# Performance work log

Measured on AMD Instinct MI355X. Metric: run time of the kernel, lower is better.

The kernel has to match this reference:

```python
import jax, jax.numpy as jnp
import numpy as np

B, T = 8, 4096
H, V, K = 512, 32000, 9


def setup_inputs() -> dict:
    key = jax.random.key(0)
    k1, k2, k3 = jax.random.split(key, 3)
    x = jax.random.randint(k1, (B, T), 0, V, dtype=jnp.int32)
    # conv1d weight [out_ch=H, in_ch=V, K], xavier-like scale
    scale = 1.0 / np.sqrt(V * K)
    W = jax.random.normal(k2, (H, V, K), dtype=jnp.float32) * scale
    b = jax.random.normal(k3, (H,), dtype=jnp.float32) * 0.01
    return {"x": x, "W": W, "b": b}


def reference(x, W, b):
    """one_hot(x, V) -> conv1d(V->H, K, pad=K//2) expressed as gather+sum.

    out[b,t,c] = bias[c] + sum_k W[c, x[b, t+k-pad], k]  (zero outside [0,T)).
    """
    Bx, Tx = x.shape
    Hh, Vv, Kk = W.shape
    pad = Kk // 2
    t = jnp.arange(Tx)
    acc = jnp.zeros((Bx, Tx, Hh), dtype=W.dtype)
    for k in range(Kk):  # small fixed kernel loop (K=9)
        src = t + (k - pad)                      # [T]
        valid = (src >= 0) & (src < Tx)          # [T]
        src_c = jnp.clip(src, 0, Tx - 1)
        ids = x[:, src_c]                        # [B,T]
        emb = jnp.take(W[:, :, k].T, ids, axis=0)  # [B,T,H] gather of column k
        acc = acc + jnp.where(valid[None, :, None], emb, jnp.zeros((), W.dtype))
    return acc + b  # [B,T,H]
```

## Files before the change

### kernel.cpp

```cpp
#include <hip/hip_runtime.h>
#include <hip/hip_bf16.h>


#define Hc 512
#define Vc 32000
#define Kc 9
#define Tc 4096
#define Bc 8
#define Mc (Vc * Kc)
#define ROWU ((Kc * Hc) / 2)
#define T_TILE 32

__device__ __forceinline__ unsigned short f2bf(float f) {
  unsigned int u = __float_as_uint(f);
  u += 0x7FFFu + ((u >> 16) & 1u);
  return (unsigned short)(u >> 16);
}

__global__ __launch_bounds__(256) void wt_transpose_kernel(
    const float* __restrict__ in, unsigned short* __restrict__ out) {
  __shared__ float tile[64][65];
  const int m0 = blockIdx.x * 64;
  const int c0 = blockIdx.y * 64;
  const int tx = threadIdx.x & 63;
  const int ty = threadIdx.x >> 6;
#pragma unroll
  for (int r = 0; r < 16; ++r) {
    const int row = ty * 16 + r;
    tile[row][tx] = in[(size_t)(c0 + row) * Mc + (m0 + tx)];
  }
  __syncthreads();
#pragma unroll
  for (int r = 0; r < 16; ++r) {
    const int mrow = ty * 16 + r;
    out[(size_t)(m0 + mrow) * Hc + (c0 + tx)] = f2bf(tile[tx][mrow]);
  }
}

__global__ __launch_bounds__(256) void conv_gather_kernel(
    const int* __restrict__ x, const unsigned int* __restrict__ Wt,
    const float* __restrict__ bias, float* __restrict__ out) {
  __shared__ int ids[T_TILE + Kc - 1];
  const int blk = blockIdx.x;
  const int b = blk >> 7;
  const int t0 = (blk & 127) * T_TILE;
  const int tid = threadIdx.x;
  if (tid < T_TILE + Kc - 1) {
    const int s = t0 + tid - (Kc / 2);
    ids[tid] = (s >= 0 && s < Tc) ? x[b * Tc + s] : Vc;
  }
  __syncthreads();
  const float2 b2 = *(const float2*)(bias + 2 * tid);
  float2* out2 = (float2*)out;
  for (int tt = 0; tt < T_TILE; ++tt) {
    float2 acc = b2;
#pragma unroll
    for (int k = 0; k < Kc; ++k) {
      const int id = ids[tt + k];
      const unsigned int w = Wt[(size_t)id * ROWU + k * (Hc / 2) + tid];
      acc.x += __uint_as_float(w << 16);
      acc.y += __uint_as_float(w & 0xFFFF0000u);
    }
    out2[(size_t)(b * Tc + t0 + tt) * (Hc / 2) + tid] = acc;
  }
}

__global__ __launch_bounds__(256) void conv_fallback_kernel(
    const int* __restrict__ x, const float* __restrict__ W,
    const float* __restrict__ bias, float* __restrict__ out) {
  const size_t idx = (size_t)blockIdx.x * 256 + threadIdx.x;
  const int c = (int)(idx & (Hc - 1));
  const size_t bt = idx >> 9;
  const int t = (int)(bt & (Tc - 1));
  const int b = (int)(bt >> 12);
  float acc = bias[c];
#pragma unroll
  for (int k = 0; k < Kc; ++k) {
    const int s = t + k - (Kc / 2);
    if (s >= 0 && s < Tc) {
      const int id = x[b * Tc + s];
      acc += W[(size_t)c * Mc + (size_t)id * Kc + k];
    }
  }
  out[idx] = acc;
}

extern "C" void kernel_launch(void* const* d_in, const int* in_sizes, int n_in,
                              void* d_out, int out_size, void* d_ws, size_t ws_size,
                              hipStream_t stream) {
  const int* x = (const int*)d_in[0];
  const float* W = (const float*)d_in[1];
  const float* bias = (const float*)d_in[2];
  float* out = (float*)d_out;

  const size_t wt_bytes = (size_t)(Vc + 1) * Kc * Hc * 2;
  if (ws_size >= wt_bytes) {
    unsigned short* Wt = (unsigned short*)d_ws;
    hipMemsetAsync(Wt + (size_t)Vc * Kc * Hc, 0, (size_t)Kc * Hc * 2, stream);
    dim3 g1(Mc / 64, Hc / 64);
    wt_transpose_kernel<<<g1, 256, 0, stream>>>(W, Wt);
    conv_gather_kernel<<<Bc * (Tc / T_TILE), 256, 0, stream>>>(
        x, (const unsigned int*)Wt, bias, out);
  } else {
    const size_t n = (size_t)Bc * Tc * Hc;
    conv_fallback_kernel<<<(int)(n / 256), 256, 0, stream>>>(x, W, bias, out);
  }
}
```

Before: 238.6 us.

## Compact transposed weights to only vocabulary ids present in input

Adds a marking pass that assigns a compact slot to each vocabulary id appearing in x, with slot 0 reserved as a zero row. The transpose kernel still reads all of W but writes bf16-packed rows only for used ids, and the gather kernel looks up ids through the slot table. The goal is to cut the write traffic of the transposed buffer and make the gathered rows denser in cache. This adds an atomic pass and extra memsets, and the mark kernel's race handling (a sentinel value followed by a plain store) relies on ordering between kernel launches.

```diff
diff --git a/kernel.cpp b/kernel.cpp
--- a/kernel.cpp
+++ b/kernel.cpp
@@ -10,6 +10,7 @@
 #define Mc (Vc * Kc)
 #define ROWU ((Kc * Hc) / 2)
 #define T_TILE 32
+#define WT_ROWS (Vc + 1)
 
 __device__ __forceinline__ unsigned short f2bf(float f) {
   unsigned int u = __float_as_uint(f);
@@ -17,8 +18,18 @@
   return (unsigned short)(u >> 16);
 }
 
+__global__ __launch_bounds__(256) void mark_kernel(
+    const int* __restrict__ x, int* __restrict__ slot, int* __restrict__ counter) {
+  const int i = blockIdx.x * 256 + threadIdx.x;
+  const int v = x[i];
+  if (atomicCAS(&slot[v], -1, -2147483647) == -1) {
+    slot[v] = 1 + atomicAdd(counter, 1);
+  }
+}
+
 __global__ __launch_bounds__(256) void wt_transpose_kernel(
-    const float* __restrict__ in, unsigned short* __restrict__ out) {
+    const float* __restrict__ in, unsigned int* __restrict__ outu,
+    const int* __restrict__ slot) {
   __shared__ float tile[64][65];
   const int m0 = blockIdx.x * 64;
   const int c0 = blockIdx.y * 64;
@@ -30,16 +41,27 @@
     tile[row][tx] = in[(size_t)(c0 + row) * Mc + (m0 + tx)];
   }
   __syncthreads();
+  const int u = threadIdx.x & 31;
+  const int rl = threadIdx.x >> 5;
 #pragma unroll
-  for (int r = 0; r < 16; ++r) {
-    const int mrow = ty * 16 + r;
-    out[(size_t)(m0 + mrow) * Hc + (c0 + tx)] = f2bf(tile[tx][mrow]);
+  for (int p = 0; p < 8; ++p) {
+    const int mrow = p * 8 + rl;
+    const int m = m0 + mrow;
+    const int v = m / Kc;
+    const int k = m - v * Kc;
+    const int s = slot[v];
+    if (s >= 0) {
+      const unsigned int val = (unsigned int)f2bf(tile[2 * u][mrow]) |
+                               ((unsigned int)f2bf(tile[2 * u + 1][mrow]) << 16);
+      outu[(size_t)s * ROWU + k * (Hc / 2) + (c0 >> 1) + u] = val;
+    }
   }
 }
 
 __global__ __launch_bounds__(256) void conv_gather_kernel(
     const int* __restrict__ x, const unsigned int* __restrict__ Wt,
-    const float* __restrict__ bias, float* __restrict__ out) {
+    const int* __restrict__ slot, const float* __restrict__ bias,
+    float* __restrict__ out) {
   __shared__ int ids[T_TILE + Kc - 1];
   const int blk = blockIdx.x;
   const int b = blk >> 7;
@@ -47,7 +69,7 @@
   const int tid = threadIdx.x;
   if (tid < T_TILE + Kc - 1) {
     const int s = t0 + tid - (Kc / 2);
-    ids[tid] = (s >= 0 && s < Tc) ? x[b * Tc + s] : Vc;
+    ids[tid] = (s >= 0 && s < Tc) ? slot[x[b * Tc + s]] : 0;
   }
   __syncthreads();
   const float2 b2 = *(const float2*)(bias + 2 * tid);
@@ -93,14 +115,23 @@
   const float* bias = (const float*)d_in[2];
   float* out = (float*)d_out;
 
-  const size_t wt_bytes = (size_t)(Vc + 1) * Kc * Hc * 2;
-  if (ws_size >= wt_bytes) {
-    unsigned short* Wt = (unsigned short*)d_ws;
-    hipMemsetAsync(Wt + (size_t)Vc * Kc * Hc, 0, (size_t)Kc * Hc * 2, stream);
+  const size_t wt_bytes = (size_t)WT_ROWS * ROWU * 4;
+  const size_t slot_off = wt_bytes;
+  const size_t cnt_off = slot_off + (size_t)Vc * 4;
+  const size_t need = cnt_off + 4;
+
+  if (ws_size >= need) {
+    unsigned int* Wt = (unsigned int*)d_ws;
+    int* slot = (int*)((char*)d_ws + slot_off);
+    int* counter = (int*)((char*)d_ws + cnt_off);
+    hipMemsetAsync(slot, 0xFF, (size_t)Vc * 4, stream);
+    hipMemsetAsync(counter, 0, 4, stream);
+    hipMemsetAsync(Wt, 0, (size_t)Kc * Hc * 2, stream);
+    mark_kernel<<<(Bc * Tc) / 256, 256, 0, stream>>>(x, slot, counter);
     dim3 g1(Mc / 64, Hc / 64);
-    wt_transpose_kernel<<<g1, 256, 0, stream>>>(W, Wt);
+    wt_transpose_kernel<<<g1, 256, 0, stream>>>(W, Wt, slot);
     conv_gather_kernel<<<Bc * (Tc / T_TILE), 256, 0, stream>>>(
-        x, (const unsigned int*)Wt, bias, out);
+        x, Wt, slot, bias, out);
   } else {
     const size_t n = (size_t)Bc * Tc * Hc;
     conv_fallback_kernel<<<(int)(n / 256), 256, 0, stream>>>(x, W, bias, out);
```

After: 234.8 us. Within noise of the previous version (-1.6%).

## Replace weight transpose and gather with token-sorted atomic scatter

Applied to the files above, without the earlier changes.

Builds a histogram, prefix scan and per-token position list, initialises the output with the bias, then for each small vocab chunk loads its weight columns into shared memory and atomically adds them into every output position that uses those tokens. This avoids materialising a transposed bf16 copy of the whole weight tensor and keeps fp32 precision. In exchange it issues on the order of a hundred million global float atomics, adds several small launches and a serial single-block scan, and still reads most of the weight tensor with strided access.

```diff
diff --git a/kernel.cpp b/kernel.cpp
--- a/kernel.cpp
+++ b/kernel.cpp
@@ -8,60 +8,105 @@
 #define Tc 4096
 #define Bc 8
 #define Mc (Vc * Kc)
-#define ROWU ((Kc * Hc) / 2)
-#define T_TILE 32
+#define VT 7
+#define NVT 4572
 
-__device__ __forceinline__ unsigned short f2bf(float f) {
-  unsigned int u = __float_as_uint(f);
-  u += 0x7FFFu + ((u >> 16) & 1u);
-  return (unsigned short)(u >> 16);
+__global__ __launch_bounds__(256) void hist_kernel(
+    const int* __restrict__ x, int* __restrict__ hist) {
+  const int i = blockIdx.x * 256 + threadIdx.x;
+  atomicAdd(&hist[x[i]], 1);
 }
 
-__global__ __launch_bounds__(256) void wt_transpose_kernel(
-    const float* __restrict__ in, unsigned short* __restrict__ out) {
-  __shared__ float tile[64][65];
-  const int m0 = blockIdx.x * 64;
+__global__ __launch_bounds__(256) void scan_kernel(
+    const int* __restrict__ hist, int* __restrict__ offs) {
+  __shared__ int wsum[4];
+  __shared__ int carry;
+  const int tid = threadIdx.x;
+  const int lane = tid & 63;
+  const int w = tid >> 6;
+  if (tid == 0) carry = 0;
+  __syncthreads();
+  for (int base = 0; base < Vc; base += 256) {
+    const int v = hist[base + tid];
+    int incl = v;
+#pragma unroll
+    for (int d = 1; d < 64; d <<= 1) {
+      const int n = __shfl_up(incl, d, 64);
+      if (lane >= d) incl += n;
+    }
+    if (lane == 63) wsum[w] = incl;
+    __syncthreads();
+    int wpref = 0;
+#pragma unroll
+    for (int q = 0; q < 3; ++q) wpref += (q < w) ? wsum[q] : 0;
+    const int c = carry;
+    offs[base + tid] = c + wpref + incl - v;
+    __syncthreads();
+    if (tid == 255) carry = c + wpref + incl;
+    __syncthreads();
+  }
+  if (tid == 0) offs[Vc] = carry;
+}
+
+__global__ __launch_bounds__(256) void fill_kernel(
+    const int* __restrict__ x, const int* __restrict__ offs,
+    int* __restrict__ cursor, int* __restrict__ list) {
+  const int i = blockIdx.x * 256 + threadIdx.x;
+  const int v = x[i];
+  const int pos = atomicAdd(&cursor[v], 1);
+  list[offs[v] + pos] = i;
+}
+
+__global__ __launch_bounds__(256) void init_out_kernel(
+    const float* __restrict__ bias, float4* __restrict__ out4) {
+  const int tid = threadIdx.x;
+  const float4 b4 = ((const float4*)bias)[tid & 127];
+  const size_t base = (size_t)blockIdx.x * 8192;
+  const int r = tid >> 7;
+#pragma unroll
+  for (int j = 0; j < 32; ++j)
+    out4[base + (size_t)(r + 2 * j) * 128 + (tid & 127)] = b4;
+}
+
+__global__ __launch_bounds__(256) void scatter_kernel(
+    const float* __restrict__ W, const int* __restrict__ offs,
+    const int* __restrict__ list, float* __restrict__ out) {
+  __shared__ float tile[63][65];
+  const int v0 = blockIdx.x * VT;
+  const int nv = (Vc - v0 < VT) ? (Vc - v0) : VT;
+  const int beg = offs[v0];
+  const int end = offs[v0 + nv];
+  if (beg == end) return;
   const int c0 = blockIdx.y * 64;
-  const int tx = threadIdx.x & 63;
-  const int ty = threadIdx.x >> 6;
+  const int tid = threadIdx.x;
+  const int tx = tid & 63;
+  const int g = tid >> 6;
+  const int m0 = v0 * Kc;
+  const int nm = nv * Kc;
+  if (tx < nm) {
+    const size_t rowbase = (size_t)(c0 + g) * Mc + m0 + tx;
 #pragma unroll
-  for (int r = 0; r < 16; ++r) {
-    const int row = ty * 16 + r;
-    tile[row][tx] = in[(size_t)(c0 + row) * Mc + (m0 + tx)];
+    for (int r = 0; r < 16; ++r) {
+      tile[tx][g + 4 * r] = W[rowbase + (size_t)(4 * r) * Mc];
+    }
   }
   __syncthreads();
+  for (int vl = 0; vl < nv; ++vl) {
+    const int b0 = offs[v0 + vl];
+    const int e0 = offs[v0 + vl + 1];
+    for (int j = b0; j < e0; ++j) {
+      const int e = list[j];
+      const int s = e & 4095;
+      const int brow = (e >> 12) * Tc;
 #pragma unroll
-  for (int r = 0; r < 16; ++r) {
-    const int mrow = ty * 16 + r;
-    out[(size_t)(m0 + mrow) * Hc + (c0 + tx)] = f2bf(tile[tx][mrow]);
-  }
-}
-
-__global__ __launch_bounds__(256) void conv_gather_kernel(
-    const int* __restrict__ x, const unsigned int* __restrict__ Wt,
-    const float* __restrict__ bias, float* __restrict__ out) {
-  __shared__ int ids[T_TILE + Kc - 1];
-  const int blk = blockIdx.x;
-  const int b = blk >> 7;
-  const int t0 = (blk & 127) * T_TILE;
-  const int tid = threadIdx.x;
-  if (tid < T_TILE + Kc - 1) {
-    const int s = t0 + tid - (Kc / 2);
-    ids[tid] = (s >= 0 && s < Tc) ? x[b * Tc + s] : Vc;
-  }
-  __syncthreads();
-  const float2 b2 = *(const float2*)(bias + 2 * tid);
-  float2* out2 = (float2*)out;
-  for (int tt = 0; tt < T_TILE; ++tt) {
-    float2 acc = b2;
-#pragma unroll
-    for (int k = 0; k < Kc; ++k) {
-      const int id = ids[tt + k];
-      const unsigned int w = Wt[(size_t)id * ROWU + k * (Hc / 2) + tid];
-      acc.x += __uint_as_float(w << 16);
-      acc.y += __uint_as_float(w & 0xFFFF0000u);
+      for (int k = g; k < Kc; k += 4) {
+        const int t = s + 4 - k;
+        if ((unsigned)t < (unsigned)Tc) {
+          atomicAdd(&out[((size_t)(brow + t) << 9) + c0 + tx],
+                    tile[vl * Kc + k][tx]);
+        }
+      }
     }
-    out2[(size_t)(b * Tc + t0 + tt) * (Hc / 2) + tid] = acc;
   }
 }
 
@@ -93,14 +138,25 @@
   const float* bias = (const float*)d_in[2];
   float* out = (float*)d_out;
 
-  const size_t wt_bytes = (size_t)(Vc + 1) * Kc * Hc * 2;
-  if (ws_size >= wt_bytes) {
-    unsigned short* Wt = (unsigned short*)d_ws;
-    hipMemsetAsync(Wt + (size_t)Vc * Kc * Hc, 0, (size_t)Kc * Hc * 2, stream);
-    dim3 g1(Mc / 64, Hc / 64);
-    wt_transpose_kernel<<<g1, 256, 0, stream>>>(W, Wt);
-    conv_gather_kernel<<<Bc * (Tc / T_TILE), 256, 0, stream>>>(
-        x, (const unsigned int*)Wt, bias, out);
+  const size_t hist_off = 0;
+  const size_t offs_off = hist_off + (size_t)Vc * 4;
+  const size_t curs_off = offs_off + (size_t)(Vc + 1) * 4;
+  const size_t list_off = curs_off + (size_t)Vc * 4;
+  const size_t need = list_off + (size_t)Bc * Tc * 4;
+
+  if (ws_size >= need) {
+    int* hist = (int*)((char*)d_ws + hist_off);
+    int* offs = (int*)((char*)d_ws + offs_off);
+    int* cursor = (int*)((char*)d_ws + curs_off);
+    int* list = (int*)((char*)d_ws + list_off);
+    hipMemsetAsync(hist, 0, (size_t)Vc * 4, stream);
+    hipMemsetAsync(cursor, 0, (size_t)Vc * 4, stream);
+    hist_kernel<<<(Bc * Tc) / 256, 256, 0, stream>>>(x, hist);
+    scan_kernel<<<1, 256, 0, stream>>>(hist, offs);
+    fill_kernel<<<(Bc * Tc) / 256, 256, 0, stream>>>(x, offs, cursor, list);
+    init_out_kernel<<<512, 256, 0, stream>>>(bias, (float4*)out);
+    dim3 g5(NVT, Hc / 64);
+    scatter_kernel<<<g5, 256, 0, stream>>>(W, offs, list, out);
   } else {
     const size_t n = (size_t)Bc * Tc * Hc;
     conv_fallback_kernel<<<(int)(n / 256), 256, 0, stream>>>(x, W, bias, out);
```

New measurement: 571.9 us. 2.4x slower.

## Replace transposed bf16 weight copy with direct scatter-accumulate conv over original layout

Applied to the files above, without the earlier changes.

Drops the per-call transpose of the full 590MB weight tensor into a bf16 workspace. Each thread now owns one output channel and reads the 9 contiguous taps W[c, id, 0..8] for each token once, scattering them into a 9-slot rotating accumulator so that each token's weights are loaded once instead of nine times. Threads in a wavefront read different channels, strided by V*K floats, so these loads are uncoalesced gathers. Accumulation stays in fp32, which removes the bf16 rounding error.

```diff
diff --git a/kernel.cpp b/kernel.cpp
--- a/kernel.cpp
+++ b/kernel.cpp
@@ -1,5 +1,4 @@
 #include <hip/hip_runtime.h>
-#include <hip/hip_bf16.h>
 
 
 #define Hc 512
@@ -8,81 +7,89 @@
 #define Tc 4096
 #define Bc 8
 #define Mc (Vc * Kc)
-#define ROWU ((Kc * Hc) / 2)
-#define T_TILE 32
 
-__device__ __forceinline__ unsigned short f2bf(float f) {
-  unsigned int u = __float_as_uint(f);
-  u += 0x7FFFu + ((u >> 16) & 1u);
-  return (unsigned short)(u >> 16);
-}
+struct F3 { float x, y, z; };
 
-__global__ __launch_bounds__(256) void wt_transpose_kernel(
-    const float* __restrict__ in, unsigned short* __restrict__ out) {
-  __shared__ float tile[64][65];
-  const int m0 = blockIdx.x * 64;
-  const int c0 = blockIdx.y * 64;
-  const int tx = threadIdx.x & 63;
-  const int ty = threadIdx.x >> 6;
+template <int PH, int KMIN, int KMAX, bool DO_STORE>
+__device__ __forceinline__ void step(const int* ids, int j,
+                                     const float* __restrict__ Wc,
+                                     float (&acc)[9], float bc, float*& outp,
+                                     bool taps_ok) {
+  if (taps_ok) {
+    const int v = ids[j];
+    const F3* p = (const F3*)(Wc + (size_t)v * Kc);
+    const F3 r0 = p[0], r1 = p[1], r2 = p[2];
+    const float w[9] = {r0.x, r0.y, r0.z, r1.x, r1.y,
+                        r1.z, r2.x, r2.y, r2.z};
 #pragma unroll
-  for (int r = 0; r < 16; ++r) {
-    const int row = ty * 16 + r;
-    tile[row][tx] = in[(size_t)(c0 + row) * Mc + (m0 + tx)];
+    for (int k = KMIN; k <= KMAX; ++k) acc[(PH - k + 9) % 9] += w[k];
   }
-  __syncthreads();
-#pragma unroll
-  for (int r = 0; r < 16; ++r) {
-    const int mrow = ty * 16 + r;
-    out[(size_t)(m0 + mrow) * Hc + (c0 + tx)] = f2bf(tile[tx][mrow]);
+  if (DO_STORE) {
+    *outp = acc[(PH + 1) % 9] + bc;
+    acc[(PH + 1) % 9] = 0.0f;
+    outp += Hc;
   }
 }
 
-__global__ __launch_bounds__(256) void conv_gather_kernel(
-    const int* __restrict__ x, const unsigned int* __restrict__ Wt,
+__global__ __launch_bounds__(256) void conv_direct_kernel(
+    const int* __restrict__ x, const float* __restrict__ W,
     const float* __restrict__ bias, float* __restrict__ out) {
-  __shared__ int ids[T_TILE + Kc - 1];
+  __shared__ int ids[72];
   const int blk = blockIdx.x;
+  const int half = blk & 1;
+  const int stripe = (blk >> 1) & 63;
   const int b = blk >> 7;
-  const int t0 = (blk & 127) * T_TILE;
+  const int t0 = stripe * 64;
   const int tid = threadIdx.x;
-  if (tid < T_TILE + Kc - 1) {
-    const int s = t0 + tid - (Kc / 2);
-    ids[tid] = (s >= 0 && s < Tc) ? x[b * Tc + s] : Vc;
+  if (tid < 72) {
+    int s = t0 - 4 + tid;
+    s = s < 0 ? 0 : (s > Tc - 1 ? Tc - 1 : s);
+    ids[tid] = x[b * Tc + s];
   }
   __syncthreads();
-  const float2 b2 = *(const float2*)(bias + 2 * tid);
-  float2* out2 = (float2*)out;
-  for (int tt = 0; tt < T_TILE; ++tt) {
-    float2 acc = b2;
-#pragma unroll
-    for (int k = 0; k < Kc; ++k) {
-      const int id = ids[tt + k];
-      const unsigned int w = Wt[(size_t)id * ROWU + k * (Hc / 2) + tid];
-      acc.x += __uint_as_float(w << 16);
-      acc.y += __uint_as_float(w & 0xFFFF0000u);
-    }
-    out2[(size_t)(b * Tc + t0 + tt) * (Hc / 2) + tid] = acc;
+  const int lane = tid & 63;
+  const int c = (half * 4 + (tid >> 6)) * 64 + lane;
+  const float* Wc = W + (size_t)c * Mc;
+  const float bc = bias[c];
+  float* outp = out + ((size_t)(b * Tc + t0) << 9) + c;
+  float acc[9] = {0, 0, 0, 0, 0, 0, 0, 0, 0};
+
+  const bool lo = (t0 != 0);
+  const bool hi = (t0 != Tc - 64);
+
+  step<0, 0, 0, false>(ids, 0, Wc, acc, bc, outp, lo);
+  step<1, 0, 1, false>(ids, 1, Wc, acc, bc, outp, lo);
+  step<2, 0, 2, false>(ids, 2, Wc, acc, bc, outp, lo);
+  step<3, 0, 3, false>(ids, 3, Wc, acc, bc, outp, lo);
+  step<4, 0, 4, false>(ids, 4, Wc, acc, bc, outp, true);
+  step<5, 0, 5, false>(ids, 5, Wc, acc, bc, outp, true);
+  step<6, 0, 6, false>(ids, 6, Wc, acc, bc, outp, true);
+  step<7, 0, 7, false>(ids, 7, Wc, acc, bc, outp, true);
+  step<8, 0, 8, true>(ids, 8, Wc, acc, bc, outp, true);
+
+#pragma unroll 1
+  for (int g = 1; g < 7; ++g) {
+    const int j0 = 9 * g;
+    step<0, 0, 8, true>(ids, j0 + 0, Wc, acc, bc, outp, true);
+    step<1, 0, 8, true>(ids, j0 + 1, Wc, acc, bc, outp, true);
+    step<2, 0, 8, true>(ids, j0 + 2, Wc, acc, bc, outp, true);
+    step<3, 0, 8, true>(ids, j0 + 3, Wc, acc, bc, outp, true);
+    step<4, 0, 8, true>(ids, j0 + 4, Wc, acc, bc, outp, true);
+    step<5, 0, 8, true>(ids, j0 + 5, Wc, acc, bc, outp, true);
+    step<6, 0, 8, true>(ids, j0 + 6, Wc, acc, bc, outp, true);
+    step<7, 0, 8, true>(ids, j0 + 7, Wc, acc, bc, outp, true);
+    step<8, 0, 8, true>(ids, j0 + 8, Wc, acc, bc, outp, true);
   }
-}
 
-__global__ __launch_bounds__(256) void conv_fallback_kernel(
-    const int* __restrict__ x, const float* __restrict__ W,
-    const float* __restrict__ bias, float* __restrict__ out) {
-  const size_t idx = (size_t)blockIdx.x * 256 + threadIdx.x;
-  const int c = (int)(idx & (Hc - 1));
-  const size_t bt = idx >> 9;
-  const int t = (int)(bt & (Tc - 1));
-  const int b = (int)(bt >> 12);
-  float acc = bias[c];
-#pragma unroll
-  for (int k = 0; k < Kc; ++k) {
-    const int s = t + k - (Kc / 2);
-    if (s >= 0 && s < Tc) {
-      const int id = x[b * Tc + s];
-      acc += W[(size_t)c * Mc + (size_t)id * Kc + k];
-    }
-  }
-  out[idx] = acc;
+  step<0, 0, 8, true>(ids, 63, Wc, acc, bc, outp, true);
+  step<1, 1, 8, true>(ids, 64, Wc, acc, bc, outp, true);
+  step<2, 2, 8, true>(ids, 65, Wc, acc, bc, outp, true);
+  step<3, 3, 8, true>(ids, 66, Wc, acc, bc, outp, true);
+  step<4, 4, 8, true>(ids, 67, Wc, acc, bc, outp, true);
+  step<5, 5, 8, true>(ids, 68, Wc, acc, bc, outp, hi);
+  step<6, 6, 8, true>(ids, 69, Wc, acc, bc, outp, hi);
+  step<7, 7, 8, true>(ids, 70, Wc, acc, bc, outp, hi);
+  step<8, 8, 8, true>(ids, 71, Wc, acc, bc, outp, hi);
 }
 
 extern "C" void kernel_launch(void* const* d_in, const int* in_sizes, int n_in,
@@ -92,17 +99,5 @@
   const float* W = (const float*)d_in[1];
   const float* bias = (const float*)d_in[2];
   float* out = (float*)d_out;
-
-  const size_t wt_bytes = (size_t)(Vc + 1) * Kc * Hc * 2;
-  if (ws_size >= wt_bytes) {
-    unsigned short* Wt = (unsigned short*)d_ws;
-    hipMemsetAsync(Wt + (size_t)Vc * Kc * Hc, 0, (size_t)Kc * Hc * 2, stream);
-    dim3 g1(Mc / 64, Hc / 64);
-    wt_transpose_kernel<<<g1, 256, 0, stream>>>(W, Wt);
-    conv_gather_kernel<<<Bc * (Tc / T_TILE), 256, 0, stream>>>(
-        x, (const unsigned int*)Wt, bias, out);
-  } else {
-    const size_t n = (size_t)Bc * Tc * Hc;
-    conv_fallback_kernel<<<(int)(n / 256), 256, 0, stream>>>(x, W, bias, out);
-  }
+  conv_direct_kernel<<<Bc * 64 * 2, 256, 0, stream>>>(x, W, bias, out);
 }
```

New measurement: 564.7 us. 137% more time.
